# Kernel optimization log

Hardware: AMD Instinct MI355X
Metric: run time of the kernel (lower is better)

The kernel has to match this reference:

```python
import jax, jax.numpy as jnp
import numpy as np

IN_DIM = 256
OUT_DIM = 256


def setup_inputs() -> dict:
    key = jax.random.key(0)
    k1, k2, k3, k4 = jax.random.split(key, 4)
    B, N = 8, 2048
    X = jax.random.normal(k1, (B, N, IN_DIM), dtype=jnp.float32)
    adj = jax.random.uniform(k2, (B, N, N), dtype=jnp.float32)
    # nn.Linear(input_dim, output_dim): W is [out, in], bias [out]
    bound = 1.0 / np.sqrt(IN_DIM)
    W = jax.random.uniform(k3, (OUT_DIM, IN_DIM), minval=-bound, maxval=bound, dtype=jnp.float32)
    b = jax.random.uniform(k4, (OUT_DIM,), minval=-bound, maxval=bound, dtype=jnp.float32)
    return {"X": X, "adj": adj, "W": W, "b": b}


def reference(X, adj, W, b):
    N = adj.shape[-1]
    # adj_hat = adj + I
    adj_hat = adj + jnp.eye(N, dtype=adj.dtype)
    # D^{-1/2} A_hat D^{-1/2}: diag matmuls are just row/col scaling
    d = jnp.sum(adj_hat, axis=-1) ** -0.5  # [B, N]
    adj_norm = d[..., :, None] * adj_hat * d[..., None, :]
    # aggregate then linear + relu
    H = jnp.matmul(adj_norm, X)  # [B, N, F_in]
    out = jnp.einsum('bnf,of->bno', H, W) + b
    return jax.nn.relu(out)
```

## Files before the change

### kernel.cpp

```cpp
#include <hip/hip_runtime.h>
#include <stdint.h>

typedef __attribute__((ext_vector_type(8))) short bf16x8;
typedef __attribute__((ext_vector_type(8))) unsigned short u16x8;
typedef __attribute__((ext_vector_type(4))) float f32x4;
typedef unsigned short u16;

constexpr int NN = 2048, NF = 256;

__device__ inline u16 f2bf(float f) {
  uint32_t u = __builtin_bit_cast(uint32_t, f);
  uint32_t r = (u + 0x7FFFu + ((u >> 16) & 1u)) >> 16;
  return (u16)r;
}
__device__ inline float bf2f(u16 h) {
  uint32_t u = ((uint32_t)h) << 16;
  return __builtin_bit_cast(float, u);
}

__device__ inline void gload_lds16(const void* g, void* l) {
  __builtin_amdgcn_global_load_lds(
      (const __attribute__((address_space(1))) uint32_t*)g,
      (__attribute__((address_space(3))) uint32_t*)l,
      16, 0, 0);
}

__global__ __launch_bounds__(256) void k_rowsum(const float* __restrict__ adj,
                                                float* __restrict__ d,
                                                const float* __restrict__ W,
                                                u16* __restrict__ Wb) {
  if (blockIdx.x >= 16384) {
    int i = (blockIdx.x - 16384) * 256 + threadIdx.x;
    float4 v = ((const float4*)W)[i];
    ushort4 o;
    o.x = f2bf(v.x); o.y = f2bf(v.y); o.z = f2bf(v.z); o.w = f2bf(v.w);
    *(ushort4*)(Wb + (size_t)i * 4) = o;
    return;
  }
  int row = blockIdx.x;
  const float4* p = (const float4*)(adj + (size_t)row * NN);
  float s = 0.f;
#pragma unroll
  for (int c = 0; c < 2; ++c) {
    float4 v = p[threadIdx.x + 256 * c];
    s += v.x + v.y + v.z + v.w;
  }
#pragma unroll
  for (int off = 32; off > 0; off >>= 1) s += __shfl_down(s, off, 64);
  __shared__ float red[4];
  int lane = threadIdx.x & 63, w = threadIdx.x >> 6;
  if (lane == 0) red[w] = s;
  __syncthreads();
  if (threadIdx.x == 0) {
    float t = red[0] + red[1] + red[2] + red[3] + 1.0f;
    d[row] = 1.0f / sqrtf(t);
  }
}

__global__ __launch_bounds__(256) void k_xprep(const float* __restrict__ X,
                                               const float* __restrict__ d,
                                               u16* __restrict__ XpT) {
  int jt = blockIdx.x, ft = blockIdx.y, b = blockIdx.z;
  int j0 = jt * 64, f0 = ft * 64;
  __shared__ u16 T[64][66];
  int t = threadIdx.x;
#pragma unroll
  for (int s = 0; s < 4; ++s) {
    int q = s * 256 + t;
    int r = q >> 4, c4 = q & 15;
    int j = j0 + r;
    float dv = d[b * NN + j];
    float4 v = *(const float4*)(X + ((size_t)(b * NN + j)) * NF + f0 + c4 * 4);
    T[r][c4 * 4 + 0] = f2bf(v.x * dv);
    T[r][c4 * 4 + 1] = f2bf(v.y * dv);
    T[r][c4 * 4 + 2] = f2bf(v.z * dv);
    T[r][c4 * 4 + 3] = f2bf(v.w * dv);
  }
  __syncthreads();
#pragma unroll
  for (int s = 0; s < 4; ++s) {
    int q = s * 256 + t;
    int fr = q >> 4, c4 = q & 15;
    ushort4 o;
    o.x = T[c4 * 4 + 0][fr]; o.y = T[c4 * 4 + 1][fr];
    o.z = T[c4 * 4 + 2][fr]; o.w = T[c4 * 4 + 3][fr];
    *(ushort4*)(XpT + ((size_t)(b * NF + f0 + fr)) * NN + j0 + c4 * 4) = o;
  }
}

#define BBASE 24576

#define MFMA8X(A0, A1, B0, B1, B2, B3)                                         \
    __builtin_amdgcn_s_setprio(1);                                             \
    acc[0][0] = __builtin_amdgcn_mfma_f32_16x16x32_bf16(A0, B0, acc[0][0], 0, 0, 0); \
    acc[0][1] = __builtin_amdgcn_mfma_f32_16x16x32_bf16(A0, B1, acc[0][1], 0, 0, 0); \
    acc[0][2] = __builtin_amdgcn_mfma_f32_16x16x32_bf16(A0, B2, acc[0][2], 0, 0, 0); \
    acc[0][3] = __builtin_amdgcn_mfma_f32_16x16x32_bf16(A0, B3, acc[0][3], 0, 0, 0); \
    acc[1][0] = __builtin_amdgcn_mfma_f32_16x16x32_bf16(A1, B0, acc[1][0], 0, 0, 0); \
    acc[1][1] = __builtin_amdgcn_mfma_f32_16x16x32_bf16(A1, B1, acc[1][1], 0, 0, 0); \
    acc[1][2] = __builtin_amdgcn_mfma_f32_16x16x32_bf16(A1, B2, acc[1][2], 0, 0, 0); \
    acc[1][3] = __builtin_amdgcn_mfma_f32_16x16x32_bf16(A1, B3, acc[1][3], 0, 0, 0); \
    __builtin_amdgcn_s_setprio(0);

#define STEP(KS, R3, W3, VMC, IA, WA, IB)                                      \
  {                                                                            \
    if (IB) {                                                                  \
      gload_lds16(b_src0 + (size_t)((KS) + 2) * 64,                            \
                  smem + BBASE + (W3) * 32768 + bw0);                          \
      gload_lds16(b_src1 + (size_t)((KS) + 2) * 64,                            \
                  smem + BBASE + (W3) * 32768 + bw1);                          \
      gload_lds16(b_src0 + (size_t)((KS) + 2) * 64 + 32,                       \
                  smem + BBASE + (W3) * 32768 + 16384 + bw0);                  \
      gload_lds16(b_src1 + (size_t)((KS) + 2) * 64 + 32,                       \
                  smem + BBASE + (W3) * 32768 + 16384 + bw1);                  \
    }                                                                          \
    if (IA) {                                                                  \
      aN0[R3] = *(const float4*)(a_gsrc + (size_t)((KS) + 3) * 64);            \
      aN1[R3] = *(const float4*)(a_gsrc + (size_t)((KS) + 3) * 64 + 4);        \
    }                                                                          \
    __builtin_amdgcn_sched_barrier(0);                                         \
    asm volatile("s_waitcnt vmcnt(" VMC ") lgkmcnt(0)" ::: "memory");          \
    __builtin_amdgcn_sched_barrier(0);                                         \
    __builtin_amdgcn_s_barrier();                                              \
    __builtin_amdgcn_sched_barrier(0);                                         \
    const char* Ab = smem + (R3) * 8192;                                       \
    const char* Be = smem + BBASE + (R3) * 32768;                              \
    const char* Bo = Be + 16384;                                               \
    bf16x8 a00 = *(const bf16x8*)(Ab + aoff0);                                 \
    bf16x8 a01 = *(const bf16x8*)(Ab + aoff0 + 1024);                          \
    bf16x8 be0 = *(const bf16x8*)(Be + boff0);                                 \
    bf16x8 be1 = *(const bf16x8*)(Be + boff0 + 1024);                          \
    bf16x8 be2 = *(const bf16x8*)(Be + boff0 + 2048);                          \
    bf16x8 be3 = *(const bf16x8*)(Be + boff0 + 3072);                          \
    __builtin_amdgcn_sched_barrier(0);                                         \
    bf16x8 a10 = *(const bf16x8*)(Ab + 4096 + aoff0);                          \
    bf16x8 a11 = *(const bf16x8*)(Ab + 4096 + aoff0 + 1024);                   \
    bf16x8 bo0 = *(const bf16x8*)(Bo + boff0);                                 \
    bf16x8 bo1 = *(const bf16x8*)(Bo + boff0 + 1024);                          \
    bf16x8 bo2 = *(const bf16x8*)(Bo + boff0 + 2048);                          \
    bf16x8 bo3 = *(const bf16x8*)(Bo + boff0 + 3072);                          \
    asm volatile("s_waitcnt lgkmcnt(6)" ::: "memory");                         \
    __builtin_amdgcn_sched_barrier(0);                                         \
    MFMA8X(a00, a01, be0, be1, be2, be3)                                       \
    __builtin_amdgcn_sched_barrier(0);                                         \
    asm volatile("s_waitcnt lgkmcnt(0)" ::: "memory");                         \
    __builtin_amdgcn_sched_barrier(0);                                         \
    MFMA8X(a10, a11, bo0, bo1, bo2, bo3)                                       \
    __builtin_amdgcn_sched_barrier(0);                                         \
    if (WA) {                                                                  \
      float4 c0 = aN0[W3], c1 = aN1[W3];                                       \
      u16x8 pk;                                                                \
      pk[0] = f2bf(c0.x); pk[1] = f2bf(c0.y); pk[2] = f2bf(c0.z);              \
      pk[3] = f2bf(c0.w); pk[4] = f2bf(c1.x); pk[5] = f2bf(c1.y);              \
      pk[6] = f2bf(c1.z); pk[7] = f2bf(c1.w);                                  \
      *(u16x8*)(smem + (W3) * 8192 + a_ldst) = pk;                             \
    }                                                                          \
    __builtin_amdgcn_sched_barrier(0);                                         \
  }

__global__ __launch_bounds__(512, 2) void k_fused(
    const float* __restrict__ adj, const u16* __restrict__ XpT,
    const float* __restrict__ dsc, const u16* __restrict__ Wb,
    const float* __restrict__ bias, float* __restrict__ out) {
  int flat = blockIdx.x;
  int b = flat & 7, mt = flat >> 3;
  int i0 = mt * 64;

  __shared__ __align__(16) char smem[122880];
  u16* Hs = (u16*)smem;

  int t = threadIdx.x;
  int lane = t & 63, w = t >> 6;
  int l15 = lane & 15, l4 = lane >> 4;
  int wr = w >> 2, wc = w & 3;

  const float* adjf = adj + ((size_t)b * NN + i0) * NN;
  const u16* XpTb = XpT + (size_t)b * NF * NN;

  int rA = t >> 3, kc = t & 7;
  const float* a_gsrc = adjf + (size_t)rA * NN + kc * 8;
  int a_ldst = (kc >> 2) * 4096 + rA * 64 + (((kc & 3) ^ ((rA >> 1) & 3)) << 4);

  int n0s = t >> 2, c0s = t & 3;
  const u16* b_src0 = XpTb + (size_t)n0s * NN + ((c0s ^ ((n0s >> 1) & 3)) << 3);
  int s1 = 512 + t;
  int n1s = s1 >> 2, c1s = s1 & 3;
  const u16* b_src1 = XpTb + (size_t)n1s * NN + ((c1s ^ ((n1s >> 1) & 3)) << 3);
  int bw0 = w << 10;
  int bw1 = 8192 + (w << 10);

  int swz = (l4 ^ ((l15 >> 1) & 3)) << 4;
  int aoff0 = wr * 2048 + l15 * 64 + swz;
  int boff0 = (wc * 64 + l15) * 64 + swz;

  f32x4 acc[2][4] = {};
  float4 aN0[3], aN1[3];

  {
    float4 p0a = *(const float4*)(a_gsrc);
    float4 p0b = *(const float4*)(a_gsrc + 4);
    float4 p1a = *(const float4*)(a_gsrc + 64);
    float4 p1b = *(const float4*)(a_gsrc + 68);
    __builtin_amdgcn_sched_barrier(0);
    gload_lds16(b_src0, smem + BBASE + bw0);
    gload_lds16(b_src1, smem + BBASE + bw1);
    gload_lds16(b_src0 + 32, smem + BBASE + 16384 + bw0);
    gload_lds16(b_src1 + 32, smem + BBASE + 16384 + bw1);
    gload_lds16(b_src0 + 64, smem + BBASE + 32768 + bw0);
    gload_lds16(b_src1 + 64, smem + BBASE + 32768 + bw1);
    gload_lds16(b_src0 + 96, smem + BBASE + 32768 + 16384 + bw0);
    gload_lds16(b_src1 + 96, smem + BBASE + 32768 + 16384 + bw1);
    __builtin_amdgcn_sched_barrier(0);
    aN0[2] = *(const float4*)(a_gsrc + 128);
    aN1[2] = *(const float4*)(a_gsrc + 132);
    __builtin_amdgcn_sched_barrier(0);
    u16x8 pk;
    pk[0] = f2bf(p0a.x); pk[1] = f2bf(p0a.y); pk[2] = f2bf(p0a.z);
    pk[3] = f2bf(p0a.w); pk[4] = f2bf(p0b.x); pk[5] = f2bf(p0b.y);
    pk[6] = f2bf(p0b.z); pk[7] = f2bf(p0b.w);
    *(u16x8*)(smem + a_ldst) = pk;
    pk[0] = f2bf(p1a.x); pk[1] = f2bf(p1a.y); pk[2] = f2bf(p1a.z);
    pk[3] = f2bf(p1a.w); pk[4] = f2bf(p1b.x); pk[5] = f2bf(p1b.y);
    pk[6] = f2bf(p1b.z); pk[7] = f2bf(p1b.w);
    *(u16x8*)(smem + 8192 + a_ldst) = pk;
    __builtin_amdgcn_sched_barrier(0);
  }

  STEP(0, 0, 2, "10", 1, 1, 1)
  STEP(1, 1, 0, "12", 1, 1, 1)
  for (int sb = 2; sb <= 23; sb += 3) {
    STEP(sb + 0, 2, 1, "12", 1, 1, 1)
    STEP(sb + 1, 0, 2, "12", 1, 1, 1)
    STEP(sb + 2, 1, 0, "12", 1, 1, 1)
  }
  STEP(26, 2, 1, "12", 1, 1, 1)
  STEP(27, 0, 2, "12", 1, 1, 1)
  STEP(28, 1, 0, "12", 1, 1, 1)
  STEP(29, 2, 1, "12", 0, 1, 1)
  STEP(30, 0, 2, "4", 0, 0, 0)
  STEP(31, 1, 0, "0", 0, 0, 0)

  __syncthreads();

  const float* db = dsc + b * NN;
#pragma unroll
  for (int mi = 0; mi < 2; ++mi) {
#pragma unroll
    for (int ni = 0; ni < 4; ++ni) {
      int f = wc * 64 + ni * 16 + l15;
      ushort4 xv = *(const ushort4*)(XpTb + (size_t)f * NN + i0 +
                                     wr * 32 + mi * 16 + l4 * 4);
#pragma unroll
      for (int qq = 0; qq < 4; ++qq) {
        int il = wr * 32 + mi * 16 + l4 * 4 + qq;
        float dv = db[i0 + il];
        float xpv = bf2f(((const u16*)&xv)[qq]);
        float hv = dv * (acc[mi][ni][qq] + xpv);
        Hs[il * 264 + f] = f2bf(hv);
      }
    }
  }
  __syncthreads();

  f32x4 acc2[2][4] = {};
#pragma unroll
  for (int kk = 0; kk < 256; kk += 32) {
    bf16x8 a2[2], b2[4];
#pragma unroll
    for (int mi = 0; mi < 2; ++mi) {
      int r = wr * 32 + mi * 16 + l15;
      a2[mi] = *(const bf16x8*)&Hs[r * 264 + kk + l4 * 8];
    }
#pragma unroll
    for (int ni = 0; ni < 4; ++ni) {
      int o = wc * 64 + ni * 16 + l15;
      b2[ni] = *(const bf16x8*)&Wb[(size_t)o * 256 + kk + l4 * 8];
    }
#pragma unroll
    for (int mi = 0; mi < 2; ++mi)
#pragma unroll
      for (int ni = 0; ni < 4; ++ni)
        acc2[mi][ni] = __builtin_amdgcn_mfma_f32_16x16x32_bf16(a2[mi], b2[ni],
                                                               acc2[mi][ni], 0, 0, 0);
  }

  float* outb = out + ((size_t)b * NN + i0) * NF;
#pragma unroll
  for (int mi = 0; mi < 2; ++mi) {
#pragma unroll
    for (int qq = 0; qq < 4; ++qq) {
      int il = wr * 32 + mi * 16 + l4 * 4 + qq;
#pragma unroll
      for (int ni = 0; ni < 4; ++ni) {
        int o = wc * 64 + ni * 16 + l15;
        float v = acc2[mi][ni][qq] + bias[o];
        outb[(size_t)il * NF + o] = fmaxf(v, 0.f);
      }
    }
  }
}

extern "C" void kernel_launch(void* const* d_in, const int* in_sizes, int n_in,
                              void* d_out, int out_size, void* d_ws, size_t ws_size,
                              hipStream_t stream) {
  const float* X    = (const float*)d_in[0];
  const float* adj  = (const float*)d_in[1];
  const float* W    = (const float*)d_in[2];
  const float* bias = (const float*)d_in[3];
  float* out = (float*)d_out;

  char* ws = (char*)d_ws;
  float* dsc = (float*)(ws);
  u16*   Wb  = (u16*)(ws + 65536);
  u16*   XpT = (u16*)(ws + 262144);

  k_rowsum<<<dim3(16448), dim3(256), 0, stream>>>(adj, dsc, W, Wb);
  k_xprep<<<dim3(32, 4, 8), dim3(256), 0, stream>>>(X, dsc, XpT);
  k_fused<<<dim3(256), dim3(512), 0, stream>>>(adj, XpT, dsc, Wb, bias, out);
}
```

Baseline: 72.22 us.

## Split K across warp rows in aggregation GEMM and reduce partials through LDS

The 8 waves switch from splitting the 64-row M tile into two halves to splitting each 64-wide K slab into two halves, so each wave computes a 64x64 tile over half of K. This cuts B-fragment LDS reads per MFMA (4 B and 4 A fragments feed 16 MFMAs). The cost is doubled accumulator registers (16 f32x4 per lane) and a cross-wave reduction through fp32 LDS plus an extra barrier. Only half the waves then run the scaling epilogue. The higher register count risks spills or lower occupancy under launch_bounds(512,2).

```diff
diff --git a/kernel.cpp b/kernel.cpp
--- a/kernel.cpp
+++ b/kernel.cpp
@@ -89,18 +89,6 @@
 }
 
 #define BBASE 24576
-
-#define MFMA8X(A0, A1, B0, B1, B2, B3)                                         \
-    __builtin_amdgcn_s_setprio(1);                                             \
-    acc[0][0] = __builtin_amdgcn_mfma_f32_16x16x32_bf16(A0, B0, acc[0][0], 0, 0, 0); \
-    acc[0][1] = __builtin_amdgcn_mfma_f32_16x16x32_bf16(A0, B1, acc[0][1], 0, 0, 0); \
-    acc[0][2] = __builtin_amdgcn_mfma_f32_16x16x32_bf16(A0, B2, acc[0][2], 0, 0, 0); \
-    acc[0][3] = __builtin_amdgcn_mfma_f32_16x16x32_bf16(A0, B3, acc[0][3], 0, 0, 0); \
-    acc[1][0] = __builtin_amdgcn_mfma_f32_16x16x32_bf16(A1, B0, acc[1][0], 0, 0, 0); \
-    acc[1][1] = __builtin_amdgcn_mfma_f32_16x16x32_bf16(A1, B1, acc[1][1], 0, 0, 0); \
-    acc[1][2] = __builtin_amdgcn_mfma_f32_16x16x32_bf16(A1, B2, acc[1][2], 0, 0, 0); \
-    acc[1][3] = __builtin_amdgcn_mfma_f32_16x16x32_bf16(A1, B3, acc[1][3], 0, 0, 0); \
-    __builtin_amdgcn_s_setprio(0);
 
 #define STEP(KS, R3, W3, VMC, IA, WA, IB)                                      \
   {                                                                            \
@@ -123,29 +111,41 @@
     __builtin_amdgcn_sched_barrier(0);                                         \
     __builtin_amdgcn_s_barrier();                                              \
     __builtin_amdgcn_sched_barrier(0);                                         \
-    const char* Ab = smem + (R3) * 8192;                                       \
-    const char* Be = smem + BBASE + (R3) * 32768;                              \
-    const char* Bo = Be + 16384;                                               \
-    bf16x8 a00 = *(const bf16x8*)(Ab + aoff0);                                 \
-    bf16x8 a01 = *(const bf16x8*)(Ab + aoff0 + 1024);                          \
-    bf16x8 be0 = *(const bf16x8*)(Be + boff0);                                 \
-    bf16x8 be1 = *(const bf16x8*)(Be + boff0 + 1024);                          \
-    bf16x8 be2 = *(const bf16x8*)(Be + boff0 + 2048);                          \
-    bf16x8 be3 = *(const bf16x8*)(Be + boff0 + 3072);                          \
-    __builtin_amdgcn_sched_barrier(0);                                         \
-    bf16x8 a10 = *(const bf16x8*)(Ab + 4096 + aoff0);                          \
-    bf16x8 a11 = *(const bf16x8*)(Ab + 4096 + aoff0 + 1024);                   \
-    bf16x8 bo0 = *(const bf16x8*)(Bo + boff0);                                 \
-    bf16x8 bo1 = *(const bf16x8*)(Bo + boff0 + 1024);                          \
-    bf16x8 bo2 = *(const bf16x8*)(Bo + boff0 + 2048);                          \
-    bf16x8 bo3 = *(const bf16x8*)(Bo + boff0 + 3072);                          \
-    asm volatile("s_waitcnt lgkmcnt(6)" ::: "memory");                         \
-    __builtin_amdgcn_sched_barrier(0);                                         \
-    MFMA8X(a00, a01, be0, be1, be2, be3)                                       \
+    const char* Ab = smem + (R3) * 8192 + awrh;                                \
+    const char* Bb = smem + BBASE + (R3) * 32768 + bwrh;                       \
+    bf16x8 af0 = *(const bf16x8*)(Ab + aoff0);                                 \
+    bf16x8 bf0 = *(const bf16x8*)(Bb + boff0);                                 \
+    bf16x8 bf1 = *(const bf16x8*)(Bb + boff0 + 1024);                          \
+    bf16x8 bf2 = *(const bf16x8*)(Bb + boff0 + 2048);                          \
+    bf16x8 bf3 = *(const bf16x8*)(Bb + boff0 + 3072);                          \
+    bf16x8 af1 = *(const bf16x8*)(Ab + aoff0 + 1024);                          \
+    bf16x8 af2 = *(const bf16x8*)(Ab + aoff0 + 2048);                          \
+    bf16x8 af3 = *(const bf16x8*)(Ab + aoff0 + 3072);                          \
+    asm volatile("s_waitcnt lgkmcnt(3)" ::: "memory");                         \
+    __builtin_amdgcn_sched_barrier(0);                                         \
+    __builtin_amdgcn_s_setprio(1);                                             \
+    acc[0][0] = __builtin_amdgcn_mfma_f32_16x16x32_bf16(af0, bf0, acc[0][0], 0, 0, 0); \
+    acc[0][1] = __builtin_amdgcn_mfma_f32_16x16x32_bf16(af0, bf1, acc[0][1], 0, 0, 0); \
+    acc[0][2] = __builtin_amdgcn_mfma_f32_16x16x32_bf16(af0, bf2, acc[0][2], 0, 0, 0); \
+    acc[0][3] = __builtin_amdgcn_mfma_f32_16x16x32_bf16(af0, bf3, acc[0][3], 0, 0, 0); \
+    __builtin_amdgcn_s_setprio(0);                                             \
     __builtin_amdgcn_sched_barrier(0);                                         \
     asm volatile("s_waitcnt lgkmcnt(0)" ::: "memory");                         \
     __builtin_amdgcn_sched_barrier(0);                                         \
-    MFMA8X(a10, a11, bo0, bo1, bo2, bo3)                                       \
+    __builtin_amdgcn_s_setprio(1);                                             \
+    acc[1][0] = __builtin_amdgcn_mfma_f32_16x16x32_bf16(af1, bf0, acc[1][0], 0, 0, 0); \
+    acc[1][1] = __builtin_amdgcn_mfma_f32_16x16x32_bf16(af1, bf1, acc[1][1], 0, 0, 0); \
+    acc[1][2] = __builtin_amdgcn_mfma_f32_16x16x32_bf16(af1, bf2, acc[1][2], 0, 0, 0); \
+    acc[1][3] = __builtin_amdgcn_mfma_f32_16x16x32_bf16(af1, bf3, acc[1][3], 0, 0, 0); \
+    acc[2][0] = __builtin_amdgcn_mfma_f32_16x16x32_bf16(af2, bf0, acc[2][0], 0, 0, 0); \
+    acc[2][1] = __builtin_amdgcn_mfma_f32_16x16x32_bf16(af2, bf1, acc[2][1], 0, 0, 0); \
+    acc[2][2] = __builtin_amdgcn_mfma_f32_16x16x32_bf16(af2, bf2, acc[2][2], 0, 0, 0); \
+    acc[2][3] = __builtin_amdgcn_mfma_f32_16x16x32_bf16(af2, bf3, acc[2][3], 0, 0, 0); \
+    acc[3][0] = __builtin_amdgcn_mfma_f32_16x16x32_bf16(af3, bf0, acc[3][0], 0, 0, 0); \
+    acc[3][1] = __builtin_amdgcn_mfma_f32_16x16x32_bf16(af3, bf1, acc[3][1], 0, 0, 0); \
+    acc[3][2] = __builtin_amdgcn_mfma_f32_16x16x32_bf16(af3, bf2, acc[3][2], 0, 0, 0); \
+    acc[3][3] = __builtin_amdgcn_mfma_f32_16x16x32_bf16(af3, bf3, acc[3][3], 0, 0, 0); \
+    __builtin_amdgcn_s_setprio(0);                                             \
     __builtin_amdgcn_sched_barrier(0);                                         \
     if (WA) {                                                                  \
       float4 c0 = aN0[W3], c1 = aN1[W3];                                       \
@@ -167,7 +167,8 @@
   int i0 = mt * 64;
 
   __shared__ __align__(16) char smem[122880];
-  u16* Hs = (u16*)smem;
+  float* Hsf = (float*)smem;
+  u16* HsBf = (u16*)(smem + 66560);
 
   int t = threadIdx.x;
   int lane = t & 63, w = t >> 6;
@@ -190,10 +191,12 @@
   int bw1 = 8192 + (w << 10);
 
   int swz = (l4 ^ ((l15 >> 1) & 3)) << 4;
-  int aoff0 = wr * 2048 + l15 * 64 + swz;
+  int aoff0 = l15 * 64 + swz;
   int boff0 = (wc * 64 + l15) * 64 + swz;
-
-  f32x4 acc[2][4] = {};
+  int awrh = wr * 4096;
+  int bwrh = wr * 16384;
+
+  f32x4 acc[4][4] = {};
   float4 aN0[3], aN1[3];
 
   {
@@ -242,21 +245,38 @@
 
   __syncthreads();
 
+  if (wr == 1) {
+#pragma unroll
+    for (int mi = 0; mi < 4; ++mi)
+#pragma unroll
+      for (int ni = 0; ni < 4; ++ni) {
+        int f = wc * 64 + ni * 16 + l15;
+#pragma unroll
+        for (int qq = 0; qq < 4; ++qq) {
+          int il = mi * 16 + l4 * 4 + qq;
+          Hsf[il * 260 + f] = acc[mi][ni][qq];
+        }
+      }
+  }
+  __syncthreads();
+
   const float* db = dsc + b * NN;
-#pragma unroll
-  for (int mi = 0; mi < 2; ++mi) {
-#pragma unroll
-    for (int ni = 0; ni < 4; ++ni) {
-      int f = wc * 64 + ni * 16 + l15;
-      ushort4 xv = *(const ushort4*)(XpTb + (size_t)f * NN + i0 +
-                                     wr * 32 + mi * 16 + l4 * 4);
-#pragma unroll
-      for (int qq = 0; qq < 4; ++qq) {
-        int il = wr * 32 + mi * 16 + l4 * 4 + qq;
-        float dv = db[i0 + il];
-        float xpv = bf2f(((const u16*)&xv)[qq]);
-        float hv = dv * (acc[mi][ni][qq] + xpv);
-        Hs[il * 264 + f] = f2bf(hv);
+  if (wr == 0) {
+#pragma unroll
+    for (int mi = 0; mi < 4; ++mi) {
+#pragma unroll
+      for (int ni = 0; ni < 4; ++ni) {
+        int f = wc * 64 + ni * 16 + l15;
+        ushort4 xv = *(const ushort4*)(XpTb + (size_t)f * NN + i0 +
+                                       mi * 16 + l4 * 4);
+#pragma unroll
+        for (int qq = 0; qq < 4; ++qq) {
+          int il = mi * 16 + l4 * 4 + qq;
+          float dv = db[i0 + il];
+          float part = acc[mi][ni][qq] + Hsf[il * 260 + f];
+          float hv = dv * (part + bf2f(((const u16*)&xv)[qq]));
+          HsBf[il * 264 + f] = f2bf(hv);
+        }
       }
     }
   }
@@ -269,7 +289,7 @@
 #pragma unroll
     for (int mi = 0; mi < 2; ++mi) {
       int r = wr * 32 + mi * 16 + l15;
-      a2[mi] = *(const bf16x8*)&Hs[r * 264 + kk + l4 * 8];
+      a2[mi] = *(const bf16x8*)&HsBf[r * 264 + kk + l4 * 8];
     }
 #pragma unroll
     for (int ni = 0; ni < 4; ++ni) {
```

After: 72.83 us. No clear change (+0.9%).
